# Optimization experiments

Measured on AMD Instinct MI355X. Metric: run time of the kernel, lower is better.

Reference implementation:

```python
import jax, jax.numpy as jnp
import numpy as np

N_NODES = 100000
N_EDGES = 1600000
D_FEAT = 128
HIDDEN = 256


def setup_inputs() -> dict:
    key = jax.random.key(0)
    k1, k2, k3, k4, k5, k6, k7 = jax.random.split(key, 7)
    h = jax.random.normal(k1, (N_NODES, D_FEAT), dtype=jnp.float32)
    src = jax.random.randint(k2, (N_EDGES,), 0, N_NODES, dtype=jnp.int64)
    dst = jax.random.randint(k3, (N_EDGES,), 0, N_NODES, dtype=jnp.int64)
    # Linear weights, torch layout: W [out, in], b [out]
    lim1 = 1.0 / np.sqrt(2 * D_FEAT)
    W1_w = jax.random.uniform(k4, (HIDDEN, 2 * D_FEAT), minval=-lim1, maxval=lim1, dtype=jnp.float32)
    W1_b = jax.random.uniform(k5, (HIDDEN,), minval=-lim1, maxval=lim1, dtype=jnp.float32)
    lim2 = 1.0 / np.sqrt(HIDDEN)
    W2_w = jax.random.uniform(k6, (1, HIDDEN), minval=-lim2, maxval=lim2, dtype=jnp.float32)
    W2_b = jax.random.uniform(k7, (1,), minval=-lim2, maxval=lim2, dtype=jnp.float32)
    return {"h": h, "src": src, "dst": dst, "W1_w": W1_w, "W1_b": W1_b, "W2_w": W2_w, "W2_b": W2_b}


def reference(h, src, dst, W1_w, W1_b, W2_w, W2_b):
    # gather per-edge src/dst node features and concat: [E, 2D]
    x = jnp.concatenate([h[src], h[dst]], axis=1)
    # Linear -> ReLU -> Linear, squeeze last dim -> [E]
    hid = jax.nn.relu(x @ W1_w.T + W1_b)          # [E, H]
    score = (hid @ W2_w.T + W2_b)[:, 0]           # [E]
    return score
```

## Files before the change

### kernel.cpp

```cpp
#include <hip/hip_runtime.h>


#define NNODES 100000
#define E_TOTAL 1600000
#define D 128
#define K2 256
#define H 256
#define NB2 49
#define EDGE_GRID 3125
#define SORT_GRID 256
#define EPB (E_TOTAL / SORT_GRID)

typedef short bf16x8 __attribute__((ext_vector_type(8)));
typedef float f32x4 __attribute__((ext_vector_type(4)));
typedef const __attribute__((address_space(1))) unsigned short* gas_t;
typedef __attribute__((address_space(3))) unsigned short* las_t;

__device__ __forceinline__ unsigned short f2bf(float f) {
    unsigned u = __float_as_uint(f);
    u += 0x7fff + ((u >> 16) & 1);
    return (unsigned short)(u >> 16);
}
__device__ __forceinline__ float bf2f(unsigned short s) {
    return __uint_as_float((unsigned)s << 16);
}

__device__ __forceinline__ int xcd_chunk(int orig, int nwg) {
    const int q = nwg >> 3, r = nwg & 7;
    const int x = orig & 7, s = orig >> 3;
    return (x < r ? x * (q + 1) : r * (q + 1) + (x - r) * q) + s;
}

__global__ void cvt_kernel(const float* __restrict__ h, const float* __restrict__ w1,
                           unsigned short* __restrict__ hbf, unsigned short* __restrict__ w1bf,
                           int n4h, int n4w, int* __restrict__ gh, int nz) {
    int i = blockIdx.x * blockDim.x + threadIdx.x;
    if (i >= n4h + n4w) {
        int z = i - (n4h + n4w);
        if (z < nz) gh[z] = 0;
        return;
    }
    const float* s; unsigned short* d; int j;
    if (i < n4h) { s = h; d = hbf; j = i; }
    else { s = w1; d = w1bf; j = i - n4h; }
    float4 v = ((const float4*)s)[j];
    ushort4 o;
    o.x = f2bf(v.x); o.y = f2bf(v.y); o.z = f2bf(v.z); o.w = f2bf(v.w);
    ((ushort4*)d)[j] = o;
}

__global__ __launch_bounds__(256, 4) void u_gemm3(
    const unsigned short* __restrict__ hbf,
    const unsigned short* __restrict__ w1bf,
    const float* __restrict__ b1,
    unsigned short* __restrict__ Us,
    unsigned short* __restrict__ Ud)
{
    __shared__ __align__(16) unsigned short A[64 * 128];

    const int tid = threadIdx.x;
    const int wave = tid >> 6;
    const int lane = tid & 63;
    const int l15 = lane & 15;
    const int quad = lane >> 4;

    const int tile = blockIdx.x >> 2;
    const int half = (blockIdx.x >> 1) & 1;
    const int nh = blockIdx.x & 1;
    const int r0 = tile * 64;
    int rows = NNODES - r0; if (rows > 64) rows = 64;
    const int koff = half * 128;
    unsigned short* U = half ? Ud : Us;

#pragma unroll
    for (int it = 0; it < 4; ++it) {
        const int s = it * 256 + tid;
        const int r = s >> 4;
        const int p = s & 15;
        const int c = p ^ (r & 15);
        if (r < rows)
            __builtin_amdgcn_global_load_lds(
                (gas_t)(hbf + (size_t)(r0 + r) * D + c * 8),
                (las_t)(A + it * 2048 + wave * 512), 16, 0, 0);
    }

    bf16x8 B[4][2];
    float bias[2];
#pragma unroll
    for (int nt = 0; nt < 2; ++nt) {
        const int n = nh * 128 + wave * 32 + nt * 16 + l15;
        bias[nt] = half ? 0.f : b1[n];
#pragma unroll
        for (int kit = 0; kit < 4; ++kit)
            B[kit][nt] = *(const bf16x8*)(w1bf + (size_t)n * K2 + koff + kit * 32 + quad * 8);
    }

    __syncthreads();

    f32x4 acc[4][2];
    const f32x4 zero = {0.f, 0.f, 0.f, 0.f};
#pragma unroll
    for (int ms = 0; ms < 4; ++ms)
#pragma unroll
        for (int nt = 0; nt < 2; ++nt)
            acc[ms][nt] = zero;

#pragma unroll
    for (int kit = 0; kit < 4; ++kit) {
        bf16x8 a[4];
#pragma unroll
        for (int ms = 0; ms < 4; ++ms) {
            const int row = ms * 16 + l15;
            const int p = (kit * 4 + quad) ^ l15;
            a[ms] = *(const bf16x8*)&A[row * 128 + p * 8];
        }
#pragma unroll
        for (int ms = 0; ms < 4; ++ms)
#pragma unroll
            for (int nt = 0; nt < 2; ++nt)
                acc[ms][nt] = __builtin_amdgcn_mfma_f32_16x16x32_bf16(
                    a[ms], B[kit][nt], acc[ms][nt], 0, 0, 0);
    }

    const int coff = nh * 128 + wave * 32 + l15 * 2;
#pragma unroll
    for (int ms = 0; ms < 4; ++ms) {
#pragma unroll
        for (int r = 0; r < 4; ++r) {
            const int m = ms * 16 + quad * 4 + r;
            if (m < rows) {
                const unsigned lo = f2bf(acc[ms][0][r] + bias[0]);
                const unsigned hi = f2bf(acc[ms][1][r] + bias[1]);
                *(unsigned*)(U + (size_t)(r0 + m) * H + coff) = lo | (hi << 16);
            }
        }
    }
}

__global__ __launch_bounds__(256) void hist49(
    const int* __restrict__ srcE, int* __restrict__ gh, int* __restrict__ bOff)
{
    __shared__ int lh[NB2];
    const int tid = threadIdx.x;
    const int base = blockIdx.x * EPB;
    if (tid < NB2) lh[tid] = 0;
    __syncthreads();
    for (int i = tid; i < EPB; i += 256)
        atomicAdd(&lh[srcE[base + i] >> 11], 1);
    __syncthreads();
    if (tid < NB2)
        bOff[blockIdx.x * NB2 + tid] = atomicAdd(&gh[tid], lh[tid]);
}

__global__ __launch_bounds__(256) void scatter49(
    const int* __restrict__ srcE, const int* __restrict__ dstE,
    const int* __restrict__ gh, const int* __restrict__ bOff,
    unsigned long long* __restrict__ pk, int* __restrict__ rank)
{
    __shared__ int pref[NB2];
    __shared__ int lcur[NB2];
    const int tid = threadIdx.x;
    const int base = blockIdx.x * EPB;
    if (tid == 0) {
        int s = 0;
        for (int b = 0; b < NB2; ++b) { pref[b] = s; s += gh[b]; }
    }
    if (tid < NB2) lcur[tid] = bOff[blockIdx.x * NB2 + tid];
    __syncthreads();
    for (int i = tid; i < EPB; i += 256) {
        const int e = base + i;
        const int s = srcE[e];
        const int d = dstE[e];
        const int b = s >> 11;
        const int r = atomicAdd(&lcur[b], 1);
        const int p = pref[b] + r;
        pk[(size_t)p] = (unsigned long long)s | ((unsigned long long)d << 17);
        rank[e] = p;
    }
}

__global__ __launch_bounds__(256) void edge_score_pk(
    const unsigned short* __restrict__ Us,
    const unsigned short* __restrict__ Ud,
    const unsigned long long* __restrict__ pk,
    const float* __restrict__ w2,
    const float* __restrict__ b2p,
    float* __restrict__ ssort)
{
    const int b = xcd_chunk(blockIdx.x, gridDim.x);
    const int tid = threadIdx.x;
    const int l = tid & 15;
    const int grp = b * 16 + (tid >> 4);

    float w2v[16];
#pragma unroll
    for (int j = 0; j < 16; ++j) {
        const int cp = l * 16 + j;
        const int n = (cp & ~31) + ((cp & 1) << 4) + ((cp & 31) >> 1);
        w2v[j] = w2[n];
    }
    const float b2 = *b2p;

    const int g0 = grp * 8;
    for (int g = g0; g < g0 + 8; ++g) {
        const int e0 = g * 4;
        const uint4 pa = *(const uint4*)(pk + e0);
        const uint4 pb = *(const uint4*)(pk + e0 + 2);
        const unsigned lo[4] = {pa.x, pa.z, pb.x, pb.z};
        const unsigned hi[4] = {pa.y, pa.w, pb.y, pb.w};
        int sv[4], dv[4];
#pragma unroll
        for (int k = 0; k < 4; ++k) {
            sv[k] = lo[k] & 0x1FFFF;
            dv[k] = ((lo[k] >> 17) | (hi[k] << 15)) & 0x1FFFF;
        }

        bf16x8 u[4][2], v[4][2];
#pragma unroll
        for (int k = 0; k < 4; ++k) {
            const bf16x8* us = (const bf16x8*)(Us + (size_t)sv[k] * H + l * 16);
            const bf16x8* ud = (const bf16x8*)(Ud + (size_t)dv[k] * H + l * 16);
            u[k][0] = us[0]; u[k][1] = us[1];
            v[k][0] = ud[0]; v[k][1] = ud[1];
        }

        float4 res;
        float* resp = (float*)&res;
#pragma unroll
        for (int k = 0; k < 4; ++k) {
            float acc = 0.f;
#pragma unroll
            for (int j = 0; j < 8; ++j) {
                float hv = bf2f((unsigned short)u[k][0][j]) + bf2f((unsigned short)v[k][0][j]);
                acc = fmaf(fmaxf(hv, 0.f), w2v[j], acc);
            }
#pragma unroll
            for (int j = 0; j < 8; ++j) {
                float hv = bf2f((unsigned short)u[k][1][j]) + bf2f((unsigned short)v[k][1][j]);
                acc = fmaf(fmaxf(hv, 0.f), w2v[j + 8], acc);
            }
            acc += __shfl_xor(acc, 1, 16);
            acc += __shfl_xor(acc, 2, 16);
            acc += __shfl_xor(acc, 4, 16);
            acc += __shfl_xor(acc, 8, 16);
            resp[k] = acc + b2;
        }
        if (l == 0) *(float4*)(ssort + e0) = res;
    }
}

__global__ __launch_bounds__(256) void unscatter(
    const float* __restrict__ ssort, const int* __restrict__ rank,
    float* __restrict__ out)
{
    const int g = blockIdx.x * 256 + threadIdx.x;
    if (g >= E_TOTAL / 4) return;
    const int e0 = g * 4;
    const int4 r4 = *(const int4*)(rank + e0);
    float4 o;
    o.x = ssort[r4.x];
    o.y = ssort[r4.y];
    o.z = ssort[r4.z];
    o.w = ssort[r4.w];
    *(float4*)(out + e0) = o;
}

__global__ __launch_bounds__(256) void edge_score(
    const unsigned short* __restrict__ Us,
    const unsigned short* __restrict__ Ud,
    const int* __restrict__ srcE,
    const int* __restrict__ dstE,
    const float* __restrict__ w2,
    const float* __restrict__ b2p,
    float* __restrict__ out)
{
    const int gt = blockIdx.x * 256 + threadIdx.x;
    const int l = gt & 15;
    const int q = gt >> 4;
    const int Q = (gridDim.x * 256) >> 4;
    const int NGRP = E_TOTAL / 4;

    float w2v[16];
#pragma unroll
    for (int j = 0; j < 16; ++j) {
        const int cp = l * 16 + j;
        const int n = (cp & ~31) + ((cp & 1) << 4) + ((cp & 31) >> 1);
        w2v[j] = w2[n];
    }
    const float b2 = *b2p;

    for (int g = q; g < NGRP; g += Q) {
        const int e0 = g * 4;
        const int4 s4 = *(const int4*)(srcE + e0);
        const int4 d4 = *(const int4*)(dstE + e0);
        const int sv[4] = {s4.x, s4.y, s4.z, s4.w};
        const int dv[4] = {d4.x, d4.y, d4.z, d4.w};

        bf16x8 u[4][2], v[4][2];
#pragma unroll
        for (int k = 0; k < 4; ++k) {
            const bf16x8* us = (const bf16x8*)(Us + (size_t)sv[k] * H + l * 16);
            const bf16x8* ud = (const bf16x8*)(Ud + (size_t)dv[k] * H + l * 16);
            u[k][0] = us[0]; u[k][1] = us[1];
            v[k][0] = ud[0]; v[k][1] = ud[1];
        }

        float4 res;
        float* resp = (float*)&res;
#pragma unroll
        for (int k = 0; k < 4; ++k) {
            float acc = 0.f;
#pragma unroll
            for (int j = 0; j < 8; ++j) {
                float hv = bf2f((unsigned short)u[k][0][j]) + bf2f((unsigned short)v[k][0][j]);
                acc = fmaf(fmaxf(hv, 0.f), w2v[j], acc);
            }
#pragma unroll
            for (int j = 0; j < 8; ++j) {
                float hv = bf2f((unsigned short)u[k][1][j]) + bf2f((unsigned short)v[k][1][j]);
                acc = fmaf(fmaxf(hv, 0.f), w2v[j + 8], acc);
            }
            acc += __shfl_xor(acc, 1, 16);
            acc += __shfl_xor(acc, 2, 16);
            acc += __shfl_xor(acc, 4, 16);
            acc += __shfl_xor(acc, 8, 16);
            resp[k] = acc + b2;
        }
        if (l == 0) *(float4*)(out + e0) = res;
    }
}


#define TILE_M 32
#define NTILES (E_TOTAL / TILE_M)
#define GRID 2500

#if defined(__has_attribute)
#if __has_attribute(amdgpu_waves_per_eu)
#define LB __launch_bounds__(256) __attribute__((amdgpu_waves_per_eu(2, 2)))
#else
#define LB __launch_bounds__(256, 2)
#endif
#else
#define LB __launch_bounds__(256, 2)
#endif

__global__ LB void edge_mlp(
    const unsigned short* __restrict__ hbf,
    const int* __restrict__ srcE,
    const int* __restrict__ dstE,
    const unsigned short* __restrict__ w1bf,
    const float* __restrict__ b1,
    const float* __restrict__ w2,
    const float* __restrict__ b2p,
    float* __restrict__ out)
{
    __shared__ __align__(16) unsigned short X[2][TILE_M * K2];
    __shared__ float red[2][TILE_M][5];

    const int tid = threadIdx.x;
    const int wave = tid >> 6;
    const int lane = tid & 63;
    const int lane15 = lane & 15;
    const int quad = lane >> 4;

    bf16x8 B[8][4];
#pragma unroll
    for (int kit = 0; kit < 8; ++kit)
#pragma unroll
        for (int nt = 0; nt < 4; ++nt) {
            int n = wave * 64 + nt * 16 + lane15;
            int k = kit * 32 + quad * 8;
            B[kit][nt] = *(const bf16x8*)(w1bf + n * K2 + k);
        }

    float b1v[4], w2v[4];
#pragma unroll
    for (int nt = 0; nt < 4; ++nt) {
        int n = wave * 64 + nt * 16 + lane15;
        b1v[nt] = b1[n];
        w2v[nt] = w2[n];
    }
    const float b2 = *b2p;

    const int r_off = tid >> 5;
    const int c = (tid & 31) ^ (r_off & 7);
    const int half = c >> 4;
    const int fc = c & 15;
    const int* idx_base = half ? dstE : srcE;
    const int gshort = fc * 8;

    const int t0 = blockIdx.x;
    int inode[4];

#pragma unroll
    for (int it = 0; it < 4; ++it)
        inode[it] = idx_base[t0 * TILE_M + it * 8 + r_off];
#pragma unroll
    for (int it = 0; it < 4; ++it)
        __builtin_amdgcn_global_load_lds(
            (gas_t)(hbf + inode[it] * D + gshort),
            (las_t)(&X[0][0] + it * 2048 + wave * 512), 16, 0, 0);
    {
        const int t1 = t0 + GRID;
#pragma unroll
        for (int it = 0; it < 4; ++it)
            inode[it] = idx_base[t1 * TILE_M + it * 8 + r_off];
    }

    int buf = 0;
    int prev_eb = -1;

    for (int tile = t0; tile < NTILES; tile += GRID) {
        __syncthreads();

        const int nt1 = tile + GRID;
        if (nt1 < NTILES) {
            unsigned short* Xn = &X[buf ^ 1][0];
#pragma unroll
            for (int it = 0; it < 4; ++it)
                __builtin_amdgcn_global_load_lds(
                    (gas_t)(hbf + inode[it] * D + gshort),
                    (las_t)(Xn + it * 2048 + wave * 512), 16, 0, 0);
        }
        const int nt2 = tile + 2 * GRID;
        if (nt2 < NTILES) {
            const int eb2 = nt2 * TILE_M;
#pragma unroll
            for (int it = 0; it < 4; ++it)
                inode[it] = idx_base[eb2 + it * 8 + r_off];
        }
        if (prev_eb >= 0 && tid < TILE_M) {
            float s = b2;
#pragma unroll
            for (int w = 0; w < 4; ++w) s += red[buf ^ 1][tid][w];
            out[prev_eb + tid] = s;
        }

        const unsigned short* Xc = &X[buf][0];
        f32x4 acc[2][4];
        const f32x4 zero = {0.f, 0.f, 0.f, 0.f};
#pragma unroll
        for (int ms = 0; ms < 2; ++ms)
#pragma unroll
            for (int nt = 0; nt < 4; ++nt)
                acc[ms][nt] = zero;

#pragma unroll
        for (int kit = 0; kit < 8; ++kit) {
            const int p8 = (((kit * 4 + quad) ^ (lane15 & 7))) * 8;
            bf16x8 a[2];
#pragma unroll
            for (int ms = 0; ms < 2; ++ms)
                a[ms] = *(const bf16x8*)&Xc[(ms * 16 + lane15) * K2 + p8];
#pragma unroll
            for (int ms = 0; ms < 2; ++ms)
#pragma unroll
                for (int nt = 0; nt < 4; ++nt)
                    acc[ms][nt] = __builtin_amdgcn_mfma_f32_16x16x32_bf16(
                        a[ms], B[kit][nt], acc[ms][nt], 0, 0, 0);
        }

#pragma unroll
        for (int ms = 0; ms < 2; ++ms)
#pragma unroll
            for (int r = 0; r < 4; ++r) {
                float p = 0.f;
#pragma unroll
                for (int nt = 0; nt < 4; ++nt) {
                    float hv = acc[ms][nt][r] + b1v[nt];
                    p = fmaf(fmaxf(hv, 0.f), w2v[nt], p);
                }
                p += __shfl_xor(p, 1, 16);
                p += __shfl_xor(p, 2, 16);
                p += __shfl_xor(p, 4, 16);
                p += __shfl_xor(p, 8, 16);
                if (lane15 == 0) red[buf][ms * 16 + quad * 4 + r][wave] = p;
            }
        prev_eb = tile * TILE_M;
        buf ^= 1;
    }

    __syncthreads();
    if (prev_eb >= 0 && tid < TILE_M) {
        float s = b2;
#pragma unroll
        for (int w = 0; w < 4; ++w) s += red[buf ^ 1][tid][w];
        out[prev_eb + tid] = s;
    }
}


extern "C" void kernel_launch(void* const* d_in, const int* in_sizes, int n_in,
                              void* d_out, int out_size, void* d_ws, size_t ws_size,
                              hipStream_t stream) {
    const float* h    = (const float*)d_in[0];
    const int*   srcE = (const int*)d_in[1];
    const int*   dstE = (const int*)d_in[2];
    const float* W1   = (const float*)d_in[3];
    const float* b1   = (const float*)d_in[4];
    const float* w2   = (const float*)d_in[5];
    const float* b2   = (const float*)d_in[6];
    float* out = (float*)d_out;

    char* ws = (char*)d_ws;
    const size_t offUs   = 0;
    const size_t offUd   = 51200000;
    const size_t offHbf  = 102400000;
    const size_t offW1bf = 128000000;
    const size_t need    = offW1bf + 131072;
    const size_t offGh   = need;
    const size_t offBO   = offGh + 4096;
    const size_t offPK   = offBO + 65536;
    const size_t need2   = offPK + 12800000;

    if (ws_size >= need) {
        unsigned short* Us   = (unsigned short*)(ws + offUs);
        unsigned short* Ud   = (unsigned short*)(ws + offUd);
        unsigned short* hbf  = (unsigned short*)(ws + offHbf);
        unsigned short* w1bf = (unsigned short*)(ws + offW1bf);
        const bool sorted = (ws_size >= need2);
        int* gh  = (int*)(ws + offGh);
        int* bO  = (int*)(ws + offBO);
        unsigned long long* pk = (unsigned long long*)(ws + offPK);
        int*   rank  = (int*)(ws + offHbf);
        float* ssort = (float*)(ws + offHbf + 6400000);

        int n4h = NNODES * D / 4, n4w = H * K2 / 4;
        const int nz = sorted ? NB2 : 0;
        cvt_kernel<<<(n4h + n4w + nz + 255) / 256, 256, 0, stream>>>(
            h, W1, hbf, w1bf, n4h, n4w, gh, nz);
        u_gemm3<<<4 * ((NNODES + 63) / 64), 256, 0, stream>>>(hbf, w1bf, b1, Us, Ud);
        if (sorted) {
            hist49<<<SORT_GRID, 256, 0, stream>>>(srcE, gh, bO);
            scatter49<<<SORT_GRID, 256, 0, stream>>>(srcE, dstE, gh, bO, pk, rank);
            edge_score_pk<<<EDGE_GRID, 256, 0, stream>>>(Us, Ud, pk, w2, b2, ssort);
            unscatter<<<(E_TOTAL / 4 + 255) / 256, 256, 0, stream>>>(ssort, rank, out);
        } else {
            edge_score<<<4096, 256, 0, stream>>>(Us, Ud, srcE, dstE, w2, b2, out);
        }
    } else {
        unsigned short* hbf  = (unsigned short*)d_ws;
        unsigned short* w1bf = hbf + (size_t)NNODES * D;
        int n4h = NNODES * D / 4, n4w = H * K2 / 4;
        cvt_kernel<<<(n4h + n4w + 255) / 256, 256, 0, stream>>>(
            h, W1, hbf, w1bf, n4h, n4w, nullptr, 0);
        edge_mlp<<<GRID, 256, 0, stream>>>(hbf, srcE, dstE, w1bf, b1, w2, b2, out);
    }
}
```

Measured before the change: 335.7 us.

## Fuse histogram into convert kernel, compute deterministic offsets in scatter, enlarge GEMM tile

The separate histogram kernel is folded into extra blocks of the bf16 convert launch. Those blocks write per-block bucket counts instead of doing global atomics, and scatter49 now derives each block's offsets and the global prefix by scanning all per-block counts. This removes one kernel launch and the global atomic pass, and makes bucket order deterministic. The node-projection GEMM tile also grows from 64 to 128 rows with occupancy lowered to 3, so each loaded weight fragment is reused across more rows at the cost of more registers and LDS.

```diff
diff --git a/kernel.cpp b/kernel.cpp
--- a/kernel.cpp
+++ b/kernel.cpp
@@ -10,6 +10,7 @@
 #define EDGE_GRID 3125
 #define SORT_GRID 256
 #define EPB (E_TOTAL / SORT_GRID)
+#define GT_ROWS 128
 
 typedef short bf16x8 __attribute__((ext_vector_type(8)));
 typedef float f32x4 __attribute__((ext_vector_type(4)));
@@ -33,13 +34,23 @@
 
 __global__ void cvt_kernel(const float* __restrict__ h, const float* __restrict__ w1,
                            unsigned short* __restrict__ hbf, unsigned short* __restrict__ w1bf,
-                           int n4h, int n4w, int* __restrict__ gh, int nz) {
-    int i = blockIdx.x * blockDim.x + threadIdx.x;
-    if (i >= n4h + n4w) {
-        int z = i - (n4h + n4w);
-        if (z < nz) gh[z] = 0;
+                           int n4h, int n4w,
+                           const int* __restrict__ srcE, int* __restrict__ cnt, int nCvt) {
+    __shared__ int lh[NB2];
+    const int tid = threadIdx.x;
+    if ((int)blockIdx.x >= nCvt) {
+        const int k = blockIdx.x - nCvt;
+        const int base = k * EPB;
+        if (tid < NB2) lh[tid] = 0;
+        __syncthreads();
+        for (int i = tid; i < EPB; i += 256)
+            atomicAdd(&lh[srcE[base + i] >> 11], 1);
+        __syncthreads();
+        if (tid < NB2) cnt[k * NB2 + tid] = lh[tid];
         return;
     }
+    int i = blockIdx.x * blockDim.x + tid;
+    if (i >= n4h + n4w) return;
     const float* s; unsigned short* d; int j;
     if (i < n4h) { s = h; d = hbf; j = i; }
     else { s = w1; d = w1bf; j = i - n4h; }
@@ -49,14 +60,14 @@
     ((ushort4*)d)[j] = o;
 }
 
-__global__ __launch_bounds__(256, 4) void u_gemm3(
+__global__ __launch_bounds__(256, 3) void u_gemm4(
     const unsigned short* __restrict__ hbf,
     const unsigned short* __restrict__ w1bf,
     const float* __restrict__ b1,
     unsigned short* __restrict__ Us,
     unsigned short* __restrict__ Ud)
 {
-    __shared__ __align__(16) unsigned short A[64 * 128];
+    __shared__ __align__(16) unsigned short A[GT_ROWS * 128];
 
     const int tid = threadIdx.x;
     const int wave = tid >> 6;
@@ -67,13 +78,13 @@
     const int tile = blockIdx.x >> 2;
     const int half = (blockIdx.x >> 1) & 1;
     const int nh = blockIdx.x & 1;
-    const int r0 = tile * 64;
-    int rows = NNODES - r0; if (rows > 64) rows = 64;
+    const int r0 = tile * GT_ROWS;
+    int rows = NNODES - r0; if (rows > GT_ROWS) rows = GT_ROWS;
     const int koff = half * 128;
     unsigned short* U = half ? Ud : Us;
 
 #pragma unroll
-    for (int it = 0; it < 4; ++it) {
+    for (int it = 0; it < 8; ++it) {
         const int s = it * 256 + tid;
         const int r = s >> 4;
         const int p = s & 15;
@@ -97,34 +108,31 @@
 
     __syncthreads();
 
-    f32x4 acc[4][2];
+    f32x4 acc[8][2];
     const f32x4 zero = {0.f, 0.f, 0.f, 0.f};
 #pragma unroll
-    for (int ms = 0; ms < 4; ++ms)
+    for (int ms = 0; ms < 8; ++ms)
 #pragma unroll
         for (int nt = 0; nt < 2; ++nt)
             acc[ms][nt] = zero;
 
 #pragma unroll
     for (int kit = 0; kit < 4; ++kit) {
-        bf16x8 a[4];
-#pragma unroll
-        for (int ms = 0; ms < 4; ++ms) {
+        const int p = (kit * 4 + quad) ^ l15;
+#pragma unroll
+        for (int ms = 0; ms < 8; ++ms) {
             const int row = ms * 16 + l15;
-            const int p = (kit * 4 + quad) ^ l15;
-            a[ms] = *(const bf16x8*)&A[row * 128 + p * 8];
-        }
-#pragma unroll
-        for (int ms = 0; ms < 4; ++ms)
+            const bf16x8 a = *(const bf16x8*)&A[row * 128 + p * 8];
 #pragma unroll
             for (int nt = 0; nt < 2; ++nt)
                 acc[ms][nt] = __builtin_amdgcn_mfma_f32_16x16x32_bf16(
-                    a[ms], B[kit][nt], acc[ms][nt], 0, 0, 0);
+                    a, B[kit][nt], acc[ms][nt], 0, 0, 0);
+        }
     }
 
     const int coff = nh * 128 + wave * 32 + l15 * 2;
 #pragma unroll
-    for (int ms = 0; ms < 4; ++ms) {
+    for (int ms = 0; ms < 8; ++ms) {
 #pragma unroll
         for (int r = 0; r < 4; ++r) {
             const int m = ms * 16 + quad * 4 + r;
@@ -137,43 +145,42 @@
     }
 }
 
-__global__ __launch_bounds__(256) void hist49(
-    const int* __restrict__ srcE, int* __restrict__ gh, int* __restrict__ bOff)
-{
-    __shared__ int lh[NB2];
-    const int tid = threadIdx.x;
-    const int base = blockIdx.x * EPB;
-    if (tid < NB2) lh[tid] = 0;
-    __syncthreads();
-    for (int i = tid; i < EPB; i += 256)
-        atomicAdd(&lh[srcE[base + i] >> 11], 1);
-    __syncthreads();
-    if (tid < NB2)
-        bOff[blockIdx.x * NB2 + tid] = atomicAdd(&gh[tid], lh[tid]);
-}
-
 __global__ __launch_bounds__(256) void scatter49(
     const int* __restrict__ srcE, const int* __restrict__ dstE,
-    const int* __restrict__ gh, const int* __restrict__ bOff,
+    const int* __restrict__ cnt,
     unsigned long long* __restrict__ pk, int* __restrict__ rank)
 {
     __shared__ int pref[NB2];
     __shared__ int lcur[NB2];
     const int tid = threadIdx.x;
-    const int base = blockIdx.x * EPB;
+    const int k = blockIdx.x;
+    const int base = k * EPB;
+
+    if (tid < NB2) {
+        int lb = 0, tot = 0;
+        for (int kk = 0; kk < SORT_GRID; ++kk) {
+            const int c = cnt[kk * NB2 + tid];
+            if (kk < k) lb += c;
+            tot += c;
+        }
+        lcur[tid] = lb;
+        pref[tid] = tot;
+    }
+    __syncthreads();
     if (tid == 0) {
         int s = 0;
-        for (int b = 0; b < NB2; ++b) { pref[b] = s; s += gh[b]; }
-    }
-    if (tid < NB2) lcur[tid] = bOff[blockIdx.x * NB2 + tid];
+        for (int b = 0; b < NB2; ++b) { const int t = pref[b]; pref[b] = s; s += t; }
+    }
     __syncthreads();
+    if (tid < NB2) lcur[tid] += pref[tid];
+    __syncthreads();
+
     for (int i = tid; i < EPB; i += 256) {
         const int e = base + i;
         const int s = srcE[e];
         const int d = dstE[e];
         const int b = s >> 11;
-        const int r = atomicAdd(&lcur[b], 1);
-        const int p = pref[b] + r;
+        const int p = atomicAdd(&lcur[b], 1);
         pk[(size_t)p] = (unsigned long long)s | ((unsigned long long)d << 17);
         rank[e] = p;
     }
@@ -509,9 +516,8 @@
     const size_t offHbf  = 102400000;
     const size_t offW1bf = 128000000;
     const size_t need    = offW1bf + 131072;
-    const size_t offGh   = need;
-    const size_t offBO   = offGh + 4096;
-    const size_t offPK   = offBO + 65536;
+    const size_t offCnt  = need;
+    const size_t offPK   = offCnt + 65536;
     const size_t need2   = offPK + 12800000;
 
     if (ws_size >= need) {
@@ -520,20 +526,20 @@
         unsigned short* hbf  = (unsigned short*)(ws + offHbf);
         unsigned short* w1bf = (unsigned short*)(ws + offW1bf);
         const bool sorted = (ws_size >= need2);
-        int* gh  = (int*)(ws + offGh);
-        int* bO  = (int*)(ws + offBO);
+        int* cnt = (int*)(ws + offCnt);
         unsigned long long* pk = (unsigned long long*)(ws + offPK);
         int*   rank  = (int*)(ws + offHbf);
         float* ssort = (float*)(ws + offHbf + 6400000);
 
         int n4h = NNODES * D / 4, n4w = H * K2 / 4;
-        const int nz = sorted ? NB2 : 0;
-        cvt_kernel<<<(n4h + n4w + nz + 255) / 256, 256, 0, stream>>>(
-            h, W1, hbf, w1bf, n4h, n4w, gh, nz);
-        u_gemm3<<<4 * ((NNODES + 63) / 64), 256, 0, stream>>>(hbf, w1bf, b1, Us, Ud);
+        const int nCvt = (n4h + n4w + 255) / 256;
+        const int cvtGrid = nCvt + (sorted ? SORT_GRID : 0);
+        cvt_kernel<<<cvtGrid, 256, 0, stream>>>(
+            h, W1, hbf, w1bf, n4h, n4w, srcE, cnt, nCvt);
+        u_gemm4<<<4 * ((NNODES + GT_ROWS - 1) / GT_ROWS), 256, 0, stream>>>(
+            hbf, w1bf, b1, Us, Ud);
         if (sorted) {
-            hist49<<<SORT_GRID, 256, 0, stream>>>(srcE, gh, bO);
-            scatter49<<<SORT_GRID, 256, 0, stream>>>(srcE, dstE, gh, bO, pk, rank);
+            scatter49<<<SORT_GRID, 256, 0, stream>>>(srcE, dstE, cnt, pk, rank);
             edge_score_pk<<<EDGE_GRID, 256, 0, stream>>>(Us, Ud, pk, w2, b2, ssort);
             unscatter<<<(E_TOTAL / 4 + 255) / 256, 256, 0, stream>>>(ssort, rank, out);
         } else {
@@ -544,7 +550,7 @@
         unsigned short* w1bf = hbf + (size_t)NNODES * D;
         int n4h = NNODES * D / 4, n4w = H * K2 / 4;
         cvt_kernel<<<(n4h + n4w + 255) / 256, 256, 0, stream>>>(
-            h, W1, hbf, w1bf, n4h, n4w, nullptr, 0);
+            h, W1, hbf, w1bf, n4h, n4w, nullptr, nullptr, (n4h + n4w + 255) / 256);
         edge_mlp<<<GRID, 256, 0, stream>>>(hbf, srcE, dstE, w1bf, b1, w2, b2, out);
     }
 }
```

Result: no change. 335.7 us (-0.0%).
